# Kernel optimization log

Measured on AMD Instinct MI355X. Metric: run time of the kernel, lower is better.

## Reference

```python
import jax, jax.numpy as jnp
import numpy as np

WS = 10      # window_size
HID = 32     # hidden_dim
B, T = 1024, 4096


def setup_inputs() -> dict:
    key = jax.random.key(0)
    k = jax.random.split(key, 7)
    returns = jax.random.normal(k[0], (B, T), dtype=jnp.float32) * 0.01
    W1 = jax.random.normal(k[1], (WS, HID), dtype=jnp.float32) * (1.0 / np.sqrt(WS))
    b1 = jnp.zeros((HID,), dtype=jnp.float32)
    W2 = jax.random.normal(k[2], (HID, HID), dtype=jnp.float32) * (1.0 / np.sqrt(HID))
    b2 = jnp.zeros((HID,), dtype=jnp.float32)
    W3 = jax.random.normal(k[3], (HID, 1), dtype=jnp.float32) * (1.0 / np.sqrt(HID))
    b3 = jnp.zeros((1,), dtype=jnp.float32)
    return {"returns": returns, "W1": W1, "b1": b1, "W2": W2, "b2": b2, "W3": W3, "b3": b3}


def reference(returns, W1, b1, W2, b2, W3, b3):
    ws = W1.shape[0]
    Bb, Tt = returns.shape
    # Unfold all sliding windows at once: windows[b, i, :] = returns[b, i:i+ws]
    # (window ending just before timestep t = i + ws)
    idx = jnp.arange(Tt - ws)[:, None] + jnp.arange(ws)[None, :]  # [T-ws, ws]
    windows = returns[:, idx]                                     # [B, T-ws, ws]
    h = jax.nn.relu(windows @ W1 + b1)                            # [B, T-ws, HID]
    h = jax.nn.relu(h @ W2 + b2)                                  # [B, T-ws, HID]
    out = 0.5 * jax.nn.sigmoid((h @ W3 + b3).squeeze(-1))         # [B, T-ws]
    # H_local[:, t] = out[:, t-ws] for t >= ws; first ws columns copy column ws
    head = jnp.broadcast_to(out[:, :1], (Bb, ws))                 # [B, ws]
    return jnp.concatenate([head, out], axis=1)                   # [B, T]
```

## Files before the change

### kernel.cpp

```cpp
#include <hip/hip_runtime.h>
#include <math.h>

typedef _Float16 f16x8 __attribute__((ext_vector_type(8)));
typedef _Float16 h2v   __attribute__((ext_vector_type(2)));
typedef float    f32x4 __attribute__((ext_vector_type(4)));
typedef __fp16   h2a   __attribute__((ext_vector_type(2)));
typedef unsigned u32x4 __attribute__((ext_vector_type(4)));

#define WS    10
#define HID   32
#define BDIM  256
#define NWAVE 4
#define GN    16
#define T_LEN 4096
#define NGRP  (T_LEN / GN)
#define PADN  4104

__device__ inline unsigned pack2u(float a, float b) {
    h2a t = __builtin_amdgcn_cvt_pkrtz(a, b);
    return __builtin_bit_cast(unsigned, t);
}
__device__ inline unsigned relu2(unsigned u) {
    h2v x = __builtin_bit_cast(h2v, u);
    h2v z = {(_Float16)0.0f, (_Float16)0.0f};
    return __builtin_bit_cast(unsigned, __builtin_elementwise_max(x, z));
}

__device__ inline int sigma(int j) {
    const int q = j >> 3, u = j & 7;
    return (u < 4) ? (4 * q + u) : (16 + 4 * q + (u - 4));
}

__global__ __launch_bounds__(BDIM, 4)
void hurst_mfma16(const float* __restrict__ returns,
                  const float* __restrict__ W1, const float* __restrict__ b1,
                  const float* __restrict__ W2, const float* __restrict__ b2,
                  const float* __restrict__ W3, const float* __restrict__ b3,
                  float* __restrict__ out)
{
    __shared__ __align__(16) _Float16 sbuf[2 * PADN];

    const int tid  = threadIdx.x;
    const int wid  = tid >> 6;
    const int lane = tid & 63;
    const int c    = lane & 15;
    const int q    = lane >> 4;

    f32x4 b1va, b1vb, b2va, b2vb, b3v;
    #pragma unroll
    for (int r = 0; r < 4; ++r) {
        b1va[r] = b1[4 * q + r];
        b1vb[r] = b1[16 + 4 * q + r];
        b2va[r] = b2[4 * q + r];
        b2vb[r] = b2[16 + 4 * q + r];
        b3v[r]  = b3[0];
    }

    f16x8 a1a, a1b, a2a, a2b, a3;
    #pragma unroll
    for (int jj = 0; jj < 8; ++jj) {
        const int k = 8 * q + jj;
        a1a[jj] = (k < WS) ? (_Float16)W1[k * HID + c]        : (_Float16)0.0f;
        a1b[jj] = (k < WS) ? (_Float16)W1[k * HID + 16 + c]   : (_Float16)0.0f;
        const int s = sigma(k);
        a2a[jj] = (_Float16)W2[s * HID + c];
        a2b[jj] = (_Float16)W2[s * HID + 16 + c];
        a3[jj]  = (_Float16)W3[s];
    }

    const float* rp   = returns + (size_t)blockIdx.x * T_LEN;
    float*       optr = out     + (size_t)blockIdx.x * T_LEN;

    {
        float f[17];
        __builtin_memcpy(f, rp + 16 * tid, 64);
        const int nx = 16 * tid + 16;
        f[16] = rp[(nx < T_LEN) ? nx : (T_LEN - 1)];
        u32x4 q0a, q0b, q1a, q1b;
        #pragma unroll
        for (int k = 0; k < 4; ++k) {
            q0a[k] = pack2u(f[2 * k],     f[2 * k + 1]);
            q0b[k] = pack2u(f[8 + 2 * k], f[9 + 2 * k]);
            q1a[k] = pack2u(f[2 * k + 1], f[2 * k + 2]);
            q1b[k] = pack2u(f[9 + 2 * k], f[10 + 2 * k]);
        }
        unsigned* s32 = (unsigned*)sbuf;
        *(u32x4*)(s32 + 8 * tid)                  = q0a;
        *(u32x4*)(s32 + 8 * tid + 4)              = q0b;
        *(u32x4*)(s32 + (PADN / 2) + 8 * tid)     = q1a;
        *(u32x4*)(s32 + (PADN / 2) + 8 * tid + 4) = q1b;
    }
    __syncthreads();

    for (int g = wid; g < NGRP; g += NWAVE) {
        const int tg = g * GN + c;
        const int ws = (tg >= WS) ? (tg - WS) : 0;

        const unsigned eoff = (ws & 1) ? (unsigned)(PADN + ws - 1) : (unsigned)ws;
        u32x4 qv;
        __builtin_memcpy(&qv, (const char*)sbuf + 2 * (eoff + ((q == 1) ? 8u : 0u)), 16);
        u32x4 xu;
        xu[0] = (q < 2) ? qv[0] : 0u;
        xu[1] = (q == 0) ? qv[1] : 0u;
        xu[2] = (q == 0) ? qv[2] : 0u;
        xu[3] = (q == 0) ? qv[3] : 0u;
        const f16x8 xb = __builtin_bit_cast(f16x8, xu);

        const f32x4 d1a = __builtin_amdgcn_mfma_f32_16x16x32_f16(a1a, xb, b1va, 0, 0, 0);
        const f32x4 d1b = __builtin_amdgcn_mfma_f32_16x16x32_f16(a1b, xb, b1vb, 0, 0, 0);

        u32x4 p1;
        p1[0] = relu2(pack2u(d1a[0], d1a[1]));
        p1[1] = relu2(pack2u(d1a[2], d1a[3]));
        p1[2] = relu2(pack2u(d1b[0], d1b[1]));
        p1[3] = relu2(pack2u(d1b[2], d1b[3]));
        const f16x8 h1 = __builtin_bit_cast(f16x8, p1);

        const f32x4 d2a = __builtin_amdgcn_mfma_f32_16x16x32_f16(a2a, h1, b2va, 0, 0, 0);
        const f32x4 d2b = __builtin_amdgcn_mfma_f32_16x16x32_f16(a2b, h1, b2vb, 0, 0, 0);

        u32x4 p2;
        p2[0] = relu2(pack2u(d2a[0], d2a[1]));
        p2[1] = relu2(pack2u(d2a[2], d2a[3]));
        p2[2] = relu2(pack2u(d2b[0], d2b[1]));
        p2[3] = relu2(pack2u(d2b[2], d2b[3]));
        const f16x8 h2 = __builtin_bit_cast(f16x8, p2);

        const f32x4 d3 = __builtin_amdgcn_mfma_f32_16x16x32_f16(a3, h2, b3v, 0, 0, 0);

        const float o = 0.5f * __builtin_amdgcn_rcpf(1.0f + __expf(-d3[0]));
        if (q == 0)
            optr[tg] = o;
    }
}

extern "C" void kernel_launch(void* const* d_in, const int* in_sizes, int n_in,
                              void* d_out, int out_size, void* d_ws, size_t ws_size,
                              hipStream_t stream) {
    const float* returns = (const float*)d_in[0];
    const float* W1      = (const float*)d_in[1];
    const float* b1      = (const float*)d_in[2];
    const float* W2      = (const float*)d_in[3];
    const float* b2      = (const float*)d_in[4];
    const float* W3      = (const float*)d_in[5];
    const float* b3      = (const float*)d_in[6];
    float* out = (float*)d_out;

    const int B = out_size / T_LEN;

    dim3 grid(B, 1, 1);
    dim3 block(BDIM, 1, 1);
    hurst_mfma16<<<grid, block, 0, stream>>>(returns, W1, b1, W2, b2, W3, b3, out);
}
```

Measured before the change: 111.3 us.

## Replace per-row LDS staging with grid-stride flat groups loading windows from global

Drops the per-block shared-memory staging of a whole row (fp16 packed, even/odd shifted copies) and the barrier that follows it. Each wave now processes flat 16-timestep groups across all rows in a persistent grid-stride loop over a fixed 1536-block grid, loading each window directly from global memory via overlapping float4 reads that rely on L1/L2 for reuse. This removes the LDS writes and the sync and raises the occupancy hint to 6 blocks per SM. The cost is redundant, unaligned global loads per lane, and the batch size of 1024 is now hardcoded.

```diff
diff --git a/kernel.cpp b/kernel.cpp
--- a/kernel.cpp
+++ b/kernel.cpp
@@ -7,14 +7,16 @@
 typedef __fp16   h2a   __attribute__((ext_vector_type(2)));
 typedef unsigned u32x4 __attribute__((ext_vector_type(4)));
 
-#define WS    10
-#define HID   32
-#define BDIM  256
-#define NWAVE 4
-#define GN    16
-#define T_LEN 4096
-#define NGRP  (T_LEN / GN)
-#define PADN  4104
+#define WS     10
+#define HID    32
+#define BDIM   256
+#define NWAVE  4
+#define GN     16
+#define T_LEN  4096
+#define GPR    (T_LEN / GN)
+#define NGTOT  (GPR * 1024)
+#define GRID   1536
+#define GSTRIDE (GRID * NWAVE)
 
 __device__ inline unsigned pack2u(float a, float b) {
     h2a t = __builtin_amdgcn_cvt_pkrtz(a, b);
@@ -31,15 +33,13 @@
     return (u < 4) ? (4 * q + u) : (16 + 4 * q + (u - 4));
 }
 
-__global__ __launch_bounds__(BDIM, 4)
-void hurst_mfma16(const float* __restrict__ returns,
+__global__ __launch_bounds__(BDIM, 6)
+void hurst_flat16(const float* __restrict__ returns,
                   const float* __restrict__ W1, const float* __restrict__ b1,
                   const float* __restrict__ W2, const float* __restrict__ b2,
                   const float* __restrict__ W3, const float* __restrict__ b3,
                   float* __restrict__ out)
 {
-    __shared__ __align__(16) _Float16 sbuf[2 * PADN];
-
     const int tid  = threadIdx.x;
     const int wid  = tid >> 6;
     const int lane = tid & 63;
@@ -60,50 +60,32 @@
     #pragma unroll
     for (int jj = 0; jj < 8; ++jj) {
         const int k = 8 * q + jj;
-        a1a[jj] = (k < WS) ? (_Float16)W1[k * HID + c]        : (_Float16)0.0f;
-        a1b[jj] = (k < WS) ? (_Float16)W1[k * HID + 16 + c]   : (_Float16)0.0f;
+        a1a[jj] = (k < WS) ? (_Float16)W1[k * HID + c]      : (_Float16)0.0f;
+        a1b[jj] = (k < WS) ? (_Float16)W1[k * HID + 16 + c] : (_Float16)0.0f;
         const int s = sigma(k);
         a2a[jj] = (_Float16)W2[s * HID + c];
         a2b[jj] = (_Float16)W2[s * HID + 16 + c];
         a3[jj]  = (_Float16)W3[s];
     }
 
-    const float* rp   = returns + (size_t)blockIdx.x * T_LEN;
-    float*       optr = out     + (size_t)blockIdx.x * T_LEN;
+    const int g0 = blockIdx.x * NWAVE + wid;
 
-    {
-        float f[17];
-        __builtin_memcpy(f, rp + 16 * tid, 64);
-        const int nx = 16 * tid + 16;
-        f[16] = rp[(nx < T_LEN) ? nx : (T_LEN - 1)];
-        u32x4 q0a, q0b, q1a, q1b;
-        #pragma unroll
-        for (int k = 0; k < 4; ++k) {
-            q0a[k] = pack2u(f[2 * k],     f[2 * k + 1]);
-            q0b[k] = pack2u(f[8 + 2 * k], f[9 + 2 * k]);
-            q1a[k] = pack2u(f[2 * k + 1], f[2 * k + 2]);
-            q1b[k] = pack2u(f[9 + 2 * k], f[10 + 2 * k]);
-        }
-        unsigned* s32 = (unsigned*)sbuf;
-        *(u32x4*)(s32 + 8 * tid)                  = q0a;
-        *(u32x4*)(s32 + 8 * tid + 4)              = q0b;
-        *(u32x4*)(s32 + (PADN / 2) + 8 * tid)     = q1a;
-        *(u32x4*)(s32 + (PADN / 2) + 8 * tid + 4) = q1b;
-    }
-    __syncthreads();
+    for (int g = g0; g < NGTOT; g += GSTRIDE) {
+        const int    row = g >> 8;
+        const int    tg  = (g & (GPR - 1)) * GN + c;
+        const int    ws  = (tg >= WS) ? (tg - WS) : 0;
+        const float* rp  = returns + (size_t)row * T_LEN;
 
-    for (int g = wid; g < NGRP; g += NWAVE) {
-        const int tg = g * GN + c;
-        const int ws = (tg >= WS) ? (tg - WS) : 0;
+        float L0[4], L1[4];
+        __builtin_memcpy(L0, rp + ws + ((q == 1) ? 6 : 0), 16);
+        __builtin_memcpy(L1, rp + ws + 4, 16);
 
-        const unsigned eoff = (ws & 1) ? (unsigned)(PADN + ws - 1) : (unsigned)ws;
-        u32x4 qv;
-        __builtin_memcpy(&qv, (const char*)sbuf + 2 * (eoff + ((q == 1) ? 8u : 0u)), 16);
         u32x4 xu;
-        xu[0] = (q < 2) ? qv[0] : 0u;
-        xu[1] = (q == 0) ? qv[1] : 0u;
-        xu[2] = (q == 0) ? qv[2] : 0u;
-        xu[3] = (q == 0) ? qv[3] : 0u;
+        xu[0] = (q == 0) ? pack2u(L0[0], L0[1])
+              : ((q == 1) ? pack2u(L0[2], L0[3]) : 0u);
+        xu[1] = (q == 0) ? pack2u(L0[2], L0[3]) : 0u;
+        xu[2] = (q == 0) ? pack2u(L1[0], L1[1]) : 0u;
+        xu[3] = (q == 0) ? pack2u(L1[2], L1[3]) : 0u;
         const f16x8 xb = __builtin_bit_cast(f16x8, xu);
 
         const f32x4 d1a = __builtin_amdgcn_mfma_f32_16x16x32_f16(a1a, xb, b1va, 0, 0, 0);
@@ -130,7 +112,7 @@
 
         const float o = 0.5f * __builtin_amdgcn_rcpf(1.0f + __expf(-d3[0]));
         if (q == 0)
-            optr[tg] = o;
+            out[(size_t)row * T_LEN + tg] = o;
     }
 }
 
@@ -146,9 +128,7 @@
     const float* b3      = (const float*)d_in[6];
     float* out = (float*)d_out;
 
-    const int B = out_size / T_LEN;
-
-    dim3 grid(B, 1, 1);
+    dim3 grid(GRID, 1, 1);
     dim3 block(BDIM, 1, 1);
-    hurst_mfma16<<<grid, block, 0, stream>>>(returns, W1, b1, W2, b2, W3, b3, out);
+    hurst_flat16<<<grid, block, 0, stream>>>(returns, W1, b1, W2, b2, W3, b3, out);
 }
```

Result: slower. 119.5 us (+7.4%).
